# Optimization experiments

Measured on AMD Instinct MI355X. Metric: run time of the kernel, lower is better.

The kernel has to match this reference:

```python
import jax, jax.numpy as jnp
import numpy as np

D_MODEL = 1024
NUM_HEADS = 16
HEAD_DIM = D_MODEL // NUM_HEADS
B, S = 4, 2048
NEG = -1e10


def setup_inputs() -> dict:
    key = jax.random.key(0)
    ks = jax.random.split(key, 10)
    s = 1.0 / np.sqrt(D_MODEL)
    x = jax.random.normal(ks[0], (B, S, D_MODEL), dtype=jnp.float32)
    mask = jnp.ones((B, S, S), dtype=jnp.int32)
    Wq = jax.random.uniform(ks[1], (D_MODEL, D_MODEL), jnp.float32, -s, s)
    bq = jnp.zeros((D_MODEL,), jnp.float32)
    Wk = jax.random.uniform(ks[2], (D_MODEL, D_MODEL), jnp.float32, -s, s)
    bk = jnp.zeros((D_MODEL,), jnp.float32)
    Wv = jax.random.uniform(ks[3], (D_MODEL, D_MODEL), jnp.float32, -s, s)
    bv = jnp.zeros((D_MODEL,), jnp.float32)
    Wo = jax.random.uniform(ks[4], (D_MODEL, D_MODEL), jnp.float32, -s, s)
    bo = jnp.zeros((D_MODEL,), jnp.float32)
    return {"x": x, "mask": mask, "Wq": Wq, "bq": bq, "Wk": Wk, "bk": bk,
            "Wv": Wv, "bv": bv, "Wo": Wo, "bo": bo}


def reference(x, mask, Wq, bq, Wk, bk, Wv, bv, Wo, bo):
    # x: [B,S,D]; projections then split into heads -> [B,H,S,hd]
    def split_heads(t):
        return t.reshape(B, S, NUM_HEADS, HEAD_DIM).transpose(0, 2, 1, 3)

    q = split_heads(x @ Wq + bq)
    k = split_heads(x @ Wk + bk)
    v = split_heads(x @ Wv + bv)
    scale = jnp.sqrt(jnp.float32(HEAD_DIM))
    # energy: [B,H,S,S]
    energy = jnp.einsum('bhqd,bhkd->bhqk', q, k) / scale
    energy = jnp.where(mask[:, None, :, :] == 0, jnp.float32(NEG), energy)
    attn = jax.nn.softmax(energy, axis=-1)
    # dropout is identity in eval mode
    out = jnp.einsum('bhqk,bhkd->bhqd', attn, v)
    out = out.transpose(0, 2, 1, 3).reshape(B, S, D_MODEL)
    return out @ Wo + bo
```

## Files before the change

### kernel.cpp

```cpp
#include <hip/hip_runtime.h>
#include <stdint.h>


#define SS 2048
#define NH 16

typedef __bf16 bf16x8 __attribute__((ext_vector_type(8)));
typedef float f32x4 __attribute__((ext_vector_type(4)));

__device__ __forceinline__ unsigned short f2bf(float f) {
  union { float f; unsigned int u; } v; v.f = f;
  unsigned int u = v.u;
  return (unsigned short)((u + 0x7fffu + ((u >> 16) & 1u)) >> 16);
}

__device__ __forceinline__ unsigned int cvtpk(float a, float b) {
  unsigned int r;
  asm("v_cvt_pk_bf16_f32 %0, %1, %2" : "=v"(r) : "v"(a), "v"(b));
  return r;
}

__device__ __forceinline__ float ex2(float x) {
  float r; asm("v_exp_f32 %0, %1" : "=v"(r) : "v"(x)); return r;
}

__device__ __forceinline__ void swap32(unsigned int& a, unsigned int& b) {
  asm volatile("v_permlane32_swap_b32 %0, %1" : "+v"(a), "+v"(b));
}
__device__ __forceinline__ void swap16(unsigned int& a, unsigned int& b) {
  asm volatile("v_permlane16_swap_b32 %0, %1" : "+v"(a), "+v"(b));
}

__device__ __forceinline__ void gload_lds16(const void* g, void* l) {
  __builtin_amdgcn_global_load_lds(
      (__attribute__((address_space(1))) void*)(void*)g,
      (__attribute__((address_space(3))) void*)l,
      16, 0, 0);
}

__global__ __launch_bounds__(256) void k_conv_x(const float* __restrict__ x,
                                                unsigned short* __restrict__ xb) {
  long i = ((long)blockIdx.x * 256 + threadIdx.x) * 4;
  float4 v = *(const float4*)(x + i);
  uint2 o;
  o.x = cvtpk(v.x, v.y);
  o.y = cvtpk(v.z, v.w);
  *(uint2*)(xb + i) = o;
}

__global__ __launch_bounds__(256) void k_transW(const float* __restrict__ W0,
                                                const float* __restrict__ W1,
                                                const float* __restrict__ W2,
                                                const float* __restrict__ W3,
                                                unsigned short* __restrict__ Wt) {
  const float* W = blockIdx.z == 0 ? W0 : blockIdx.z == 1 ? W1 : blockIdx.z == 2 ? W2 : W3;
  unsigned short* dst = Wt + (size_t)blockIdx.z * 1024 * 1024;
  __shared__ float t[64][65];
  int r0 = blockIdx.y * 64, c0 = blockIdx.x * 64;
  int tr = threadIdx.x >> 6, tc = threadIdx.x & 63;
#pragma unroll
  for (int i = 0; i < 16; i++) {
    int r = tr + i * 4;
    t[r][tc] = W[(size_t)(r0 + r) * 1024 + c0 + tc];
  }
  __syncthreads();
#pragma unroll
  for (int i = 0; i < 16; i++) {
    int r = tr + i * 4;
    dst[(size_t)(c0 + r) * 1024 + r0 + tc] = f2bf(t[tc][r]);
  }
}

__global__ __launch_bounds__(256) void k_maskflags(const int* __restrict__ mask,
                                                   int* __restrict__ flg) {
  int kt = blockIdx.x, qb = blockIdx.y, b = blockIdx.z;
  const int* M = mask + ((size_t)b * SS + qb * 128) * SS + kt * 64;
  int tid = threadIdx.x;
  int ok = 1;
#pragma unroll
  for (int i = 0; i < 8; i++) {
    int r = (tid >> 4) + i * 16;
    int4 v = *(const int4*)(M + (size_t)r * SS + (tid & 15) * 4);
    ok &= (v.x != 0) & (v.y != 0) & (v.z != 0) & (v.w != 0);
  }
  ok = __all(ok) ? 1 : 0;
  __shared__ int s[4];
  if ((tid & 63) == 0) s[tid >> 6] = ok;
  __syncthreads();
  if (tid == 0) flg[((size_t)b * 16 + qb) * 32 + kt] = s[0] & s[1] & s[2] & s[3];
}

template <int EPI>
__global__ __launch_bounds__(256) void k_gemm(const unsigned short* __restrict__ A,
                                              const unsigned short* __restrict__ Bt,
                                              const float* __restrict__ bias,
                                              void* __restrict__ Cout, float scale) {
  constexpr int K = 1024, N = 1024;
  __shared__ unsigned short lA[128 * 64];
  __shared__ unsigned short lB[128 * 64];
  const int tid = threadIdx.x;
  const int lane = tid & 63, wave = tid >> 6;
  const int wr = wave >> 1, wc = wave & 1;
  const int g = lane >> 4, c = lane & 15;

  const int bid = blockIdx.x;
  const int xcd = bid & 7, idx = bid >> 3;
  const int by = xcd * 8 + (idx >> 3), bx = idx & 7;
  const long brow = (long)by * 128, bcol = (long)bx * 128;

  f32x4 acc[4][4] = {};

  int sr[4], sch[4];
#pragma unroll
  for (int j = 0; j < 4; j++) {
    int p = j * 4096 + tid * 16;
    int r = p >> 7;
    int sl = (p >> 4) & 7;
    sr[j] = r;
    sch[j] = (sl ^ (r & 7)) * 8;
  }
  char* lbaseA = (char*)lA + wave * 1024;
  char* lbaseB = (char*)lB + wave * 1024;

  for (int k0 = 0; k0 < K; k0 += 64) {
#pragma unroll
    for (int j = 0; j < 4; j++) {
      gload_lds16(A + (brow + sr[j]) * K + k0 + sch[j], lbaseA + j * 4096);
      gload_lds16(Bt + (bcol + sr[j]) * K + k0 + sch[j], lbaseB + j * 4096);
    }
    __syncthreads();
#pragma unroll
    for (int ks = 0; ks < 2; ks++) {
      bf16x8 af[4], bfr[4];
#pragma unroll
      for (int m = 0; m < 4; m++) {
        int ra = wr * 64 + m * 16 + c;
        af[m] = *(const bf16x8*)((const char*)lA + ra * 128 + ((ks * 64 + g * 16) ^ ((ra & 7) << 4)));
        int rb = wc * 64 + m * 16 + c;
        bfr[m] = *(const bf16x8*)((const char*)lB + rb * 128 + ((ks * 64 + g * 16) ^ ((rb & 7) << 4)));
      }
      __builtin_amdgcn_s_setprio(1);
#pragma unroll
      for (int m = 0; m < 4; m++)
#pragma unroll
        for (int n = 0; n < 4; n++)
          acc[m][n] = __builtin_amdgcn_mfma_f32_16x16x32_bf16(af[m], bfr[n], acc[m][n], 0, 0, 0);
      __builtin_amdgcn_s_setprio(0);
    }
    __syncthreads();
  }

#pragma unroll
  for (int m = 0; m < 4; m++) {
#pragma unroll
    for (int n = 0; n < 4; n++) {
      long row0 = brow + wr * 64 + m * 16 + g * 4;
      long col = bcol + wc * 64 + n * 16 + c;
      float bv = bias[col];
      if (EPI == 0) {
        unsigned short* C = (unsigned short*)Cout;
#pragma unroll
        for (int r = 0; r < 4; r++)
          C[(row0 + r) * N + col] = f2bf((acc[m][n][r] + bv) * scale);
      } else if (EPI == 1) {
        unsigned short* C = (unsigned short*)Cout;
        long b_ = row0 >> 11, s = row0 & 2047;
        size_t base = ((size_t)(b_ * NH + (col >> 6)) * 64 + (col & 63)) * SS + s;
        ushort4 pk;
        pk.x = f2bf(acc[m][n][0] + bv);
        pk.y = f2bf(acc[m][n][1] + bv);
        pk.z = f2bf(acc[m][n][2] + bv);
        pk.w = f2bf(acc[m][n][3] + bv);
        *(ushort4*)(C + base) = pk;
      } else {
        float* C = (float*)Cout;
#pragma unroll
        for (int r = 0; r < 4; r++)
          C[(row0 + r) * N + col] = acc[m][n][r] + bv;
      }
    }
  }
}

__global__ __launch_bounds__(256) void k_flash(const unsigned short* __restrict__ Q,
                                               const unsigned short* __restrict__ Kb,
                                               const unsigned short* __restrict__ Vt,
                                               const int* __restrict__ mask,
                                               const int* __restrict__ flg,
                                               unsigned short* __restrict__ O) {
  __shared__ unsigned short lK[2][4096];
  __shared__ unsigned short lV[2][4096];
  const int tid = threadIdx.x, lane = tid & 63, w = tid >> 6;
  const int g = lane >> 4, c = lane & 15;

  const int bid = blockIdx.x;
  const int xcd = bid & 7, jj = bid >> 3;
  const int qb = jj & 15, Ghi = jj >> 4;
  const int G = xcd * 8 + Ghi;
  const int h = G & 15, b = G >> 4;

  const int q0 = qb * 128 + w * 32;
  const long mrow0 = (long)b * SS + q0;

  const unsigned short* Kbase = Kb + (size_t)b * SS * 1024 + h * 64;
  const unsigned short* Vbase = Vt + (size_t)((b * NH + h) * 64) * SS;
  const int* Mbase = mask + ((size_t)b * SS + q0) * SS;
  const int* Fbase = flg + ((size_t)b * 16 + qb) * 32;

  bf16x8 qf[2][2];
#pragma unroll
  for (int rt = 0; rt < 2; rt++)
#pragma unroll
    for (int ks = 0; ks < 2; ks++)
      qf[rt][ks] = *(const bf16x8*)(Q + (mrow0 + rt * 16 + c) * 1024 + h * 64 + ks * 32 + g * 8);

  const int p0 = tid * 16;
  const int r0 = p0 >> 7;
  const int co = (((p0 >> 4) & 7) ^ (r0 & 7)) * 8;
  const unsigned short* pK0 = Kbase + (size_t)r0 * 1024 + co;
  const unsigned short* pV0 = Vbase + (size_t)r0 * SS + co;
  char* dK = (char*)&lK[0][0] + w * 1024;
  char* dV = (char*)&lV[0][0] + w * 1024;

  gload_lds16(pK0, dK);
  gload_lds16(pK0 + 32 * 1024, dK + 4096);
  gload_lds16(pV0, dV);
  gload_lds16(pV0 + 32 * (size_t)SS, dV + 4096);
  __syncthreads();

  float mst[2] = {-1e30f, -1e30f}, lst[2] = {0.0f, 0.0f};
  f32x4 o[2][4] = {};
  int cur = 0;

  for (int kt = 0; kt < SS / 64; kt++) {
    if (kt + 1 < SS / 64) {
      const unsigned short* sK = pK0 + (size_t)(kt + 1) * 64 * 1024;
      const unsigned short* sV = pV0 + (size_t)(kt + 1) * 64;
      char* tK = dK + (cur ^ 1) * 8192;
      char* tV = dV + (cur ^ 1) * 8192;
      gload_lds16(sK, tK);
      gload_lds16(sK + 32 * 1024, tK + 4096);
      gload_lds16(sV, tV);
      gload_lds16(sV + 32 * (size_t)SS, tV + 4096);
    }

    const char* bK = (const char*)&lK[0][0] + cur * 8192;
    const char* bV = (const char*)&lV[0][0] + cur * 8192;

    bf16x8 kf[4][2];
#pragma unroll
    for (int ct = 0; ct < 4; ct++)
#pragma unroll
      for (int ks = 0; ks < 2; ks++)
        kf[ct][ks] = *(const bf16x8*)(bK + (ct * 16 + c) * 128 +
                                      ((ks * 64 + g * 16) ^ ((c & 7) << 4)));

    f32x4 sc[2][4] = {};
    __builtin_amdgcn_s_setprio(1);
#pragma unroll
    for (int ks = 0; ks < 2; ks++)
#pragma unroll
      for (int rt = 0; rt < 2; rt++)
#pragma unroll
        for (int ct = 0; ct < 4; ct++)
          sc[rt][ct] = __builtin_amdgcn_mfma_f32_16x16x32_bf16(kf[ct][ks], qf[rt][ks], sc[rt][ct], 0, 0, 0);
    __builtin_amdgcn_s_setprio(0);

    if (Fbase[kt] == 0) {
      const int key0 = kt * 64;
#pragma unroll
      for (int rt = 0; rt < 2; rt++)
#pragma unroll
        for (int ct = 0; ct < 4; ct++)
#pragma unroll
          for (int r = 0; r < 4; r++) {
            int mv = Mbase[(size_t)(rt * 16 + c) * SS + key0 + ct * 16 + g * 4 + r];
            if (mv == 0) sc[rt][ct][r] = -1e10f;
          }
    }

    float tm[2];
#pragma unroll
    for (int rt = 0; rt < 2; rt++) {
      f32x4 m4 = sc[rt][0];
#pragma unroll
      for (int ct = 1; ct < 4; ct++)
#pragma unroll
        for (int r = 0; r < 4; r++) m4[r] = fmaxf(m4[r], sc[rt][ct][r]);
      float v = fmaxf(fmaxf(m4[0], m4[1]), fmaxf(m4[2], m4[3]));
      v = fmaxf(v, __shfl_xor(v, 16, 64));
      v = fmaxf(v, __shfl_xor(v, 32, 64));
      tm[rt] = v;
    }

    int need = (tm[0] > mst[0] + 8.0f) | (tm[1] > mst[1] + 8.0f);
    if (__any(need)) {
#pragma unroll
      for (int rt = 0; rt < 2; rt++) {
        float mnew = fmaxf(mst[rt], tm[rt]);
        float sf = ex2(mst[rt] - mnew);
        mst[rt] = mnew;
        lst[rt] *= sf;
#pragma unroll
        for (int ct = 0; ct < 4; ct++)
#pragma unroll
          for (int r = 0; r < 4; r++) o[rt][ct][r] *= sf;
      }
    }

    union PU { unsigned int wd[4]; bf16x8 v; };
    PU pf[2][2];
#pragma unroll
    for (int rt = 0; rt < 2; rt++) {
      f32x4 ts4 = {0.0f, 0.0f, 0.0f, 0.0f};
      unsigned int Wd[4][2];
#pragma unroll
      for (int ct = 0; ct < 4; ct++) {
        f32x4 p;
#pragma unroll
        for (int r = 0; r < 4; r++) {
          p[r] = ex2(sc[rt][ct][r] - mst[rt]);
          ts4[r] += p[r];
        }
        Wd[ct][0] = cvtpk(p[0], p[1]);
        Wd[ct][1] = cvtpk(p[2], p[3]);
      }
#pragma unroll
      for (int ks = 0; ks < 2; ks++)
#pragma unroll
        for (int hh = 0; hh < 2; hh++) {
          unsigned int a = Wd[2 * ks][hh], bb = Wd[2 * ks + 1][hh];
          swap32(a, bb);
          swap16(a, bb);
          pf[rt][ks].wd[hh] = a;
          pf[rt][ks].wd[2 + hh] = bb;
        }
      float ts = (ts4[0] + ts4[1]) + (ts4[2] + ts4[3]);
      ts += __shfl_xor(ts, 16, 64);
      ts += __shfl_xor(ts, 32, 64);
      lst[rt] += ts;
    }

    bf16x8 vf[4][2];
#pragma unroll
    for (int ct = 0; ct < 4; ct++)
#pragma unroll
      for (int ks = 0; ks < 2; ks++)
        vf[ct][ks] = *(const bf16x8*)(bV + (ct * 16 + c) * 128 +
                                      ((ks * 64 + g * 16) ^ ((c & 7) << 4)));
    __builtin_amdgcn_s_setprio(1);
#pragma unroll
    for (int rt = 0; rt < 2; rt++)
#pragma unroll
      for (int ct = 0; ct < 4; ct++)
#pragma unroll
        for (int ks = 0; ks < 2; ks++)
          o[rt][ct] = __builtin_amdgcn_mfma_f32_16x16x32_bf16(vf[ct][ks], pf[rt][ks].v, o[rt][ct], 0, 0, 0);
    __builtin_amdgcn_s_setprio(0);

    __syncthreads();
    cur ^= 1;
  }

#pragma unroll
  for (int rt = 0; rt < 2; rt++) {
    float inv = 1.0f / lst[rt];
#pragma unroll
    for (int ct = 0; ct < 4; ct++) {
      uint2 pk;
      pk.x = cvtpk(o[rt][ct][0] * inv, o[rt][ct][1] * inv);
      pk.y = cvtpk(o[rt][ct][2] * inv, o[rt][ct][3] * inv);
      *(uint2*)(O + (mrow0 + rt * 16 + c) * 1024 + h * 64 + ct * 16 + g * 4) = pk;
    }
  }
}

extern "C" void kernel_launch(void* const* d_in, const int* in_sizes, int n_in,
                              void* d_out, int out_size, void* d_ws, size_t ws_size,
                              hipStream_t stream) {
  const float* x  = (const float*)d_in[0];
  const int* mask = (const int*)d_in[1];
  const float* Wq = (const float*)d_in[2];
  const float* bq = (const float*)d_in[3];
  const float* Wk = (const float*)d_in[4];
  const float* bk = (const float*)d_in[5];
  const float* Wv = (const float*)d_in[6];
  const float* bv = (const float*)d_in[7];
  const float* Wo = (const float*)d_in[8];
  const float* bo = (const float*)d_in[9];

  char* ws = (char*)d_ws;
  unsigned short* xb = (unsigned short*)ws;
  unsigned short* Wt = (unsigned short*)(ws + (16ull << 20));
  unsigned short* Qb = (unsigned short*)(ws + (24ull << 20));
  unsigned short* Kb = (unsigned short*)(ws + (40ull << 20));
  unsigned short* Vt = (unsigned short*)(ws + (56ull << 20));
  int* flg = (int*)d_out;

  k_conv_x<<<8192, 256, 0, stream>>>(x, xb);
  k_transW<<<dim3(16, 16, 4), 256, 0, stream>>>(Wq, Wk, Wv, Wo, Wt);
  k_maskflags<<<dim3(32, 16, 4), 256, 0, stream>>>(mask, flg);
  k_gemm<0><<<512, 256, 0, stream>>>(xb, Wt, bq, Qb, 0.125f * 1.44269504088896f);
  k_gemm<0><<<512, 256, 0, stream>>>(xb, Wt + (1u << 20), bk, Kb, 1.0f);
  k_gemm<1><<<512, 256, 0, stream>>>(xb, Wt + (2u << 20), bv, Vt, 1.0f);
  k_flash<<<1024, 256, 0, stream>>>(Qb, Kb, Vt, mask, flg, xb);
  k_gemm<2><<<512, 256, 0, stream>>>(xb, Wt + (3u << 20), bo, d_out, 1.0f);
}
```

Before: 242.7 us.

## Triple-buffer K tiles, fold max offset into MFMA init, defer row-sum reduction

```diff
diff --git a/kernel.cpp b/kernel.cpp
--- a/kernel.cpp
+++ b/kernel.cpp
@@ -182,13 +182,13 @@
   }
 }
 
-__global__ __launch_bounds__(256) void k_flash(const unsigned short* __restrict__ Q,
-                                               const unsigned short* __restrict__ Kb,
-                                               const unsigned short* __restrict__ Vt,
-                                               const int* __restrict__ mask,
-                                               const int* __restrict__ flg,
-                                               unsigned short* __restrict__ O) {
-  __shared__ unsigned short lK[2][4096];
+__global__ __launch_bounds__(256, 4) void k_flash(const unsigned short* __restrict__ Q,
+                                                  const unsigned short* __restrict__ Kb,
+                                                  const unsigned short* __restrict__ Vt,
+                                                  const int* __restrict__ mask,
+                                                  const int* __restrict__ flg,
+                                                  unsigned short* __restrict__ O) {
+  __shared__ unsigned short lK[3][4096];
   __shared__ unsigned short lV[2][4096];
   const int tid = threadIdx.x, lane = tid & 63, w = tid >> 6;
   const int g = lane >> 4, c = lane & 15;
@@ -207,6 +207,11 @@
   const int* Mbase = mask + ((size_t)b * SS + q0) * SS;
   const int* Fbase = flg + ((size_t)b * 16 + qb) * 32;
 
+  int allok = 1;
+#pragma unroll
+  for (int i = 0; i < 32; i++) allok &= Fbase[i];
+  allok = __builtin_amdgcn_readfirstlane(allok);
+
   bf16x8 qf[2][2];
 #pragma unroll
   for (int rt = 0; rt < 2; rt++)
@@ -214,48 +219,58 @@
     for (int ks = 0; ks < 2; ks++)
       qf[rt][ks] = *(const bf16x8*)(Q + (mrow0 + rt * 16 + c) * 1024 + h * 64 + ks * 32 + g * 8);
 
-  const int p0 = tid * 16;
-  const int r0 = p0 >> 7;
-  const int co = (((p0 >> 4) & 7) ^ (r0 & 7)) * 8;
-  const unsigned short* pK0 = Kbase + (size_t)r0 * 1024 + co;
-  const unsigned short* pV0 = Vbase + (size_t)r0 * SS + co;
-  char* dK = (char*)&lK[0][0] + w * 1024;
-  char* dV = (char*)&lV[0][0] + w * 1024;
-
-  gload_lds16(pK0, dK);
-  gload_lds16(pK0 + 32 * 1024, dK + 4096);
-  gload_lds16(pV0, dV);
-  gload_lds16(pV0 + 32 * (size_t)SS, dV + 4096);
-  __syncthreads();
-
-  float mst[2] = {-1e30f, -1e30f}, lst[2] = {0.0f, 0.0f};
+  const int pB = tid * 16;
+  const int r0 = pB >> 7;
+  const int co = (((pB >> 4) & 7) ^ (r0 & 7)) * 8;
+  const unsigned short* gK = Kbase + (size_t)r0 * 1024 + co;
+  const unsigned short* gV = Vbase + (size_t)r0 * SS + co;
+  const int wb = w * 1024;
+
+  char* sk0 = (char*)&lK[0][0];
+  char* sk1 = (char*)&lK[1][0];
+  char* sk2 = (char*)&lK[2][0];
+  char* sv0 = (char*)&lV[0][0];
+  char* sv1 = (char*)&lV[1][0];
+
+#define STAGE_K(kt_, dst_) do { \
+    const unsigned short* aK_ = gK + (size_t)(kt_) * (64 * 1024); \
+    gload_lds16(aK_, (dst_) + wb); \
+    gload_lds16(aK_ + 32 * 1024, (dst_) + wb + 4096); } while (0)
+#define STAGE_V(kt_, dst_) do { \
+    const unsigned short* aV_ = gV + (size_t)(kt_) * 64; \
+    gload_lds16(aV_, (dst_) + wb); \
+    gload_lds16(aV_ + 32 * (size_t)SS, (dst_) + wb + 4096); } while (0)
+
+  STAGE_K(0, sk0);
+  STAGE_V(0, sv0);
+  STAGE_K(1, sk1);
+
+  float mst[2] = {8.0f, 8.0f}, lst[2] = {0.0f, 0.0f};
   f32x4 o[2][4] = {};
-  int cur = 0;
 
   for (int kt = 0; kt < SS / 64; kt++) {
-    if (kt + 1 < SS / 64) {
-      const unsigned short* sK = pK0 + (size_t)(kt + 1) * 64 * 1024;
-      const unsigned short* sV = pV0 + (size_t)(kt + 1) * 64;
-      char* tK = dK + (cur ^ 1) * 8192;
-      char* tV = dV + (cur ^ 1) * 8192;
-      gload_lds16(sK, tK);
-      gload_lds16(sK + 32 * 1024, tK + 4096);
-      gload_lds16(sV, tV);
-      gload_lds16(sV + 32 * (size_t)SS, tV + 4096);
-    }
-
-    const char* bK = (const char*)&lK[0][0] + cur * 8192;
-    const char* bV = (const char*)&lV[0][0] + cur * 8192;
+    if (kt < SS / 64 - 1) asm volatile("s_waitcnt vmcnt(2)" ::: "memory");
+    else                  asm volatile("s_waitcnt vmcnt(0)" ::: "memory");
+    __builtin_amdgcn_s_barrier();
+    __builtin_amdgcn_sched_barrier(0);
+    if (kt + 1 < SS / 64) STAGE_V(kt + 1, sv1);
+    if (kt + 2 < SS / 64) STAGE_K(kt + 2, sk2);
 
     bf16x8 kf[4][2];
 #pragma unroll
     for (int ct = 0; ct < 4; ct++)
 #pragma unroll
       for (int ks = 0; ks < 2; ks++)
-        kf[ct][ks] = *(const bf16x8*)(bK + (ct * 16 + c) * 128 +
+        kf[ct][ks] = *(const bf16x8*)(sk0 + (ct * 16 + c) * 128 +
                                       ((ks * 64 + g * 16) ^ ((c & 7) << 4)));
 
-    f32x4 sc[2][4] = {};
+    f32x4 sc[2][4];
+#pragma unroll
+    for (int rt = 0; rt < 2; rt++)
+#pragma unroll
+      for (int ct = 0; ct < 4; ct++)
+#pragma unroll
+        for (int r = 0; r < 4; r++) sc[rt][ct][r] = -mst[rt];
     __builtin_amdgcn_s_setprio(1);
 #pragma unroll
     for (int ks = 0; ks < 2; ks++)
@@ -266,7 +281,7 @@
           sc[rt][ct] = __builtin_amdgcn_mfma_f32_16x16x32_bf16(kf[ct][ks], qf[rt][ks], sc[rt][ct], 0, 0, 0);
     __builtin_amdgcn_s_setprio(0);
 
-    if (Fbase[kt] == 0) {
+    if (!allok) {
       const int key0 = kt * 64;
 #pragma unroll
       for (int rt = 0; rt < 2; rt++)
@@ -279,32 +294,29 @@
           }
     }
 
-    float tm[2];
+    float pm[2];
 #pragma unroll
     for (int rt = 0; rt < 2; rt++) {
-      f32x4 m4 = sc[rt][0];
-#pragma unroll
-      for (int ct = 1; ct < 4; ct++)
-#pragma unroll
-        for (int r = 0; r < 4; r++) m4[r] = fmaxf(m4[r], sc[rt][ct][r]);
-      float v = fmaxf(fmaxf(m4[0], m4[1]), fmaxf(m4[2], m4[3]));
-      v = fmaxf(v, __shfl_xor(v, 16, 64));
-      v = fmaxf(v, __shfl_xor(v, 32, 64));
-      tm[rt] = v;
-    }
-
-    int need = (tm[0] > mst[0] + 8.0f) | (tm[1] > mst[1] + 8.0f);
-    if (__any(need)) {
+      f32x4 m4;
+#pragma unroll
+      for (int r = 0; r < 4; r++)
+        m4[r] = fmaxf(fmaxf(sc[rt][0][r], sc[rt][1][r]), fmaxf(sc[rt][2][r], sc[rt][3][r]));
+      pm[rt] = fmaxf(fmaxf(m4[0], m4[1]), fmaxf(m4[2], m4[3]));
+    }
+    if (__any((pm[0] > 8.0f) | (pm[1] > 8.0f))) {
 #pragma unroll
       for (int rt = 0; rt < 2; rt++) {
-        float mnew = fmaxf(mst[rt], tm[rt]);
-        float sf = ex2(mst[rt] - mnew);
-        mst[rt] = mnew;
+        float tmv = pm[rt];
+        tmv = fmaxf(tmv, __shfl_xor(tmv, 16, 64));
+        tmv = fmaxf(tmv, __shfl_xor(tmv, 32, 64));
+        float dpos = fmaxf(tmv, 0.0f);
+        float sf = ex2(-dpos);
+        mst[rt] += dpos;
         lst[rt] *= sf;
 #pragma unroll
         for (int ct = 0; ct < 4; ct++)
 #pragma unroll
-          for (int r = 0; r < 4; r++) o[rt][ct][r] *= sf;
+          for (int r = 0; r < 4; r++) { o[rt][ct][r] *= sf; sc[rt][ct][r] -= dpos; }
       }
     }
 
@@ -319,7 +331,7 @@
         f32x4 p;
 #pragma unroll
         for (int r = 0; r < 4; r++) {
-          p[r] = ex2(sc[rt][ct][r] - mst[rt]);
+          p[r] = ex2(sc[rt][ct][r]);
           ts4[r] += p[r];
         }
         Wd[ct][0] = cvtpk(p[0], p[1]);
@@ -335,10 +347,7 @@
           pf[rt][ks].wd[hh] = a;
           pf[rt][ks].wd[2 + hh] = bb;
         }
-      float ts = (ts4[0] + ts4[1]) + (ts4[2] + ts4[3]);
-      ts += __shfl_xor(ts, 16, 64);
-      ts += __shfl_xor(ts, 32, 64);
-      lst[rt] += ts;
+      lst[rt] += (ts4[0] + ts4[1]) + (ts4[2] + ts4[3]);
     }
 
     bf16x8 vf[4][2];
@@ -346,7 +355,7 @@
     for (int ct = 0; ct < 4; ct++)
 #pragma unroll
       for (int ks = 0; ks < 2; ks++)
-        vf[ct][ks] = *(const bf16x8*)(bV + (ct * 16 + c) * 128 +
+        vf[ct][ks] = *(const bf16x8*)(sv0 + (ct * 16 + c) * 128 +
                                       ((ks * 64 + g * 16) ^ ((c & 7) << 4)));
     __builtin_amdgcn_s_setprio(1);
 #pragma unroll
@@ -358,13 +367,16 @@
           o[rt][ct] = __builtin_amdgcn_mfma_f32_16x16x32_bf16(vf[ct][ks], pf[rt][ks].v, o[rt][ct], 0, 0, 0);
     __builtin_amdgcn_s_setprio(0);
 
-    __syncthreads();
-    cur ^= 1;
+    char* tk = sk0; sk0 = sk1; sk1 = sk2; sk2 = tk;
+    char* tv = sv0; sv0 = sv1; sv1 = tv;
   }
 
 #pragma unroll
   for (int rt = 0; rt < 2; rt++) {
-    float inv = 1.0f / lst[rt];
+    float t = lst[rt];
+    t += __shfl_xor(t, 16, 64);
+    t += __shfl_xor(t, 32, 64);
+    float inv = 1.0f / t;
 #pragma unroll
     for (int ct = 0; ct < 4; ct++) {
       uint2 pk;
@@ -373,6 +385,8 @@
       *(uint2*)(O + (mrow0 + rt * 16 + c) * 1024 + h * 64 + ct * 16 + g * 4) = pk;
     }
   }
+#undef STAGE_K
+#undef STAGE_V
 }
 
 extern "C" void kernel_launch(void* const* d_in, const int* in_sizes, int n_in,
```

After: 210.9 us. 1.15x faster.
